# Optimization experiments

Measured on AMD Instinct MI355X. Metric: run time of the kernel, lower is better.

The kernel has to match this reference:

```python
import jax, jax.numpy as jnp
import numpy as np

N_NODES = 100000
N_EDGES = 1600000
D_IN = 128
D_HID = 128


def setup_inputs() -> dict:
    key = jax.random.key(0)
    ks = jax.random.split(key, 9)
    x = jax.random.normal(ks[0], (N_NODES, D_IN), dtype=jnp.float32)
    edge_index = jax.random.randint(ks[1], (2, N_EDGES), 0, N_NODES, dtype=jnp.int64)
    s = 1.0 / np.sqrt(D_IN)
    W0 = jax.random.uniform(ks[2], (D_IN, D_HID), jnp.float32, -s, s)
    W1 = jax.random.uniform(ks[3], (D_HID, D_HID), jnp.float32, -s, s)
    W2 = jax.random.uniform(ks[4], (D_HID, D_HID), jnp.float32, -s, s)
    b0 = jax.random.uniform(ks[5], (D_HID,), jnp.float32, -s, s)
    b1 = jax.random.uniform(ks[6], (D_HID,), jnp.float32, -s, s)
    b2 = jax.random.uniform(ks[7], (D_HID,), jnp.float32, -s, s)
    return {"x": x, "edge_index": edge_index,
            "W0": W0, "W1": W1, "W2": W2, "b0": b0, "b1": b1, "b2": b2}


def _gcn_norm(edge_index, num_nodes):
    # add self loops, compute symmetric normalization D^-1/2 (A+I) D^-1/2
    loop = jnp.arange(num_nodes, dtype=edge_index.dtype)
    src = jnp.concatenate([edge_index[0], loop])
    dst = jnp.concatenate([edge_index[1], loop])
    deg = jax.ops.segment_sum(jnp.ones_like(dst, dtype=jnp.float32), dst,
                              num_segments=num_nodes)
    dis = jnp.where(deg > 0, jax.lax.rsqrt(deg), 0.0)
    norm = dis[src] * dis[dst]  # [E+N]
    return src, dst, norm


def _gcn_conv(x, src, dst, norm, W, b, num_nodes):
    h = x @ W                           # [N, D]
    msg = h[src] * norm[:, None]        # [E+N, D]
    out = jax.ops.segment_sum(msg, dst, num_segments=num_nodes)
    return out + b


def reference(x, edge_index, W0, W1, W2, b0, b1, b2):
    n = x.shape[0]
    src, dst, norm = _gcn_norm(edge_index, n)
    h = jax.nn.relu(_gcn_conv(x, src, dst, norm, W0, b0, n))
    h = jax.nn.relu(_gcn_conv(h, src, dst, norm, W1, b1, n))
    h = jax.nn.relu(_gcn_conv(h, src, dst, norm, W2, b2, n))
    return jax.nn.log_softmax(h, axis=1)
```

## Files before the change

kernel.cpp:

```cpp
#include <hip/hip_runtime.h>
#include <cstdint>


#define D 128
#define NBMAX 800
#define ACHUNK 8192
#define QCAP 4608

typedef __attribute__((ext_vector_type(8))) short bf16x8;
typedef __attribute__((ext_vector_type(4))) float f32x4;

__device__ inline ushort f_to_bf(float f) {
    uint x = __float_as_uint(f);
    return (ushort)((x + 0x7fffu + ((x >> 16) & 1u)) >> 16);
}
__device__ inline uint pack_bf2(float a, float b) {
    return (uint)f_to_bf(a) | ((uint)f_to_bf(b) << 16);
}
__device__ inline float bf_lo(uint u) { return __uint_as_float(u << 16); }
__device__ inline float bf_hi(uint u) { return __uint_as_float(u & 0xffff0000u); }


__global__ void hist_pass(const int* __restrict__ ei, int* __restrict__ hist,
                          int* __restrict__ cursor, int E, int NB) {
    __shared__ int lh[NBMAX];
    if (blockIdx.x == 0 && threadIdx.x == 0) *cursor = 0;
    for (int i = threadIdx.x; i < NB; i += 256) lh[i] = 0;
    __syncthreads();
    int e0 = blockIdx.x * ACHUNK;
    int e1 = min(e0 + ACHUNK, E);
    for (int e = e0 + threadIdx.x; e < e1; e += 256)
        atomicAdd(&lh[ei[(size_t)E + e] >> 7], 1);
    __syncthreads();
    int* hrow = hist + (size_t)blockIdx.x * NB;
    for (int i = threadIdx.x; i < NB; i += 256) hrow[i] = lh[i];
}

__global__ void col_scan(int* __restrict__ hist, int* __restrict__ btotal,
                         int* __restrict__ bbase, int* __restrict__ cursor,
                         int B, int NB) {
    __shared__ int s[256];
    int g = blockIdx.x;
    int t = threadIdx.x;
    int v = (t < B) ? hist[(size_t)t * NB + g] : 0;
    s[t] = v;
    __syncthreads();
    for (int off = 1; off < 256; off <<= 1) {
        int u = (t >= off) ? s[t - off] : 0;
        __syncthreads();
        s[t] += u;
        __syncthreads();
    }
    if (t < B) hist[(size_t)t * NB + g] = s[t] - v;
    if (t == 255) {
        btotal[g] = s[255];
        bbase[g] = atomicAdd(cursor, s[255]);
    }
}

__global__ void scatter_pass(const int* __restrict__ ei, const int* __restrict__ hist,
                             const int* __restrict__ bbase, uint* __restrict__ queue,
                             int E, int NB) {
    __shared__ int loff[NBMAX];
    const int* hrow = hist + (size_t)blockIdx.x * NB;
    for (int i = threadIdx.x; i < NB; i += 256) loff[i] = bbase[i] + hrow[i];
    __syncthreads();
    int e0 = blockIdx.x * ACHUNK;
    int e1 = min(e0 + ACHUNK, E);
    for (int e = e0 + threadIdx.x; e < e1; e += 256) {
        int d = ei[(size_t)E + e];
        int s = ei[e];
        int slot = atomicAdd(&loff[d >> 7], 1);
        queue[slot] = ((uint)(d & 127) << 17) | (uint)s;
    }
}

__global__ void finalize_pass(const uint* __restrict__ queue, const int* __restrict__ bbase,
                              const int* __restrict__ btotal, int2* __restrict__ bd,
                              float* __restrict__ dis, int* __restrict__ col, int N) {
    __shared__ uint qs[QCAP];
    __shared__ int cnt[128], pre[128], run[128];
    int g = blockIdx.x;
    int t = threadIdx.x;
    int base = bbase[g], m = btotal[g];
    bool fits = (m <= QCAP);
    if (t < 128) { cnt[t] = 0; run[t] = 0; }
    __syncthreads();
    for (int i = t; i < m; i += 256) {
        uint e = queue[base + i];
        if (fits) qs[i] = e;
        atomicAdd(&cnt[e >> 17], 1);
    }
    __syncthreads();
    if (t < 128) pre[t] = cnt[t];
    __syncthreads();
    for (int off = 1; off < 128; off <<= 1) {
        int u = (t < 128 && t >= off) ? pre[t - off] : 0;
        __syncthreads();
        if (t < 128) pre[t] += u;
        __syncthreads();
    }
    if (t < 128) {
        int node = (g << 7) + t;
        if (node < N) {
            bd[node] = make_int2(base + pre[t] - cnt[t], cnt[t]);
            dis[node] = rsqrtf((float)(cnt[t] + 1));
        }
    }
    __syncthreads();
    for (int i = t; i < m; i += 256) {
        uint e = fits ? qs[i] : queue[base + i];
        int idx = (int)(e >> 17);
        int r = atomicAdd(&run[idx], 1);
        col[base + pre[idx] - cnt[idx] + r] = (int)(e & 0x1FFFFu);
    }
}

__global__ void convert_w3(const float* __restrict__ W0, const float* __restrict__ W1,
                           const float* __restrict__ W2, ushort* __restrict__ Wt0,
                           ushort* __restrict__ Wt1, ushort* __restrict__ Wt2) {
    int which = blockIdx.x >> 6;
    int i = (blockIdx.x & 63) * 256 + threadIdx.x;
    const float* W = which == 0 ? W0 : (which == 1 ? W1 : W2);
    ushort* Wt = which == 0 ? Wt0 : (which == 1 ? Wt1 : Wt2);
    int k = i >> 7, nn = i & 127;
    Wt[nn * D + k] = f_to_bf(W[i]);
}

template <int F32IN>
__global__ __launch_bounds__(256)
void gemm_mfma(const void* __restrict__ Xv, const ushort* __restrict__ Wt,
               const float* __restrict__ dis, ushort* __restrict__ G, int n) {
    __shared__ ushort Bs[32 * 64 * 8];
    int tid = threadIdx.x;
    int wave = tid >> 6, lane = tid & 63;
    int lr = lane & 15, quad = lane >> 4;
    int rowbase = blockIdx.x * 128 + wave * 32;

    for (int s = tid; s < 2048; s += 256) {
        int g = s >> 6, l = s & 63;
        int kk = g >> 3, nt = g & 7;
        int srow = nt * 16 + (l & 15);
        int scol = kk * 32 + (l >> 4) * 8;
        ((uint4*)Bs)[s] = *(const uint4*)(Wt + srow * D + scol);
    }
    __syncthreads();

    int ar0 = min(rowbase + lr, n - 1);
    int ar1 = min(rowbase + 16 + lr, n - 1);

    f32x4 acc[2][8];
#pragma unroll
    for (int rt = 0; rt < 2; rt++)
#pragma unroll
        for (int nt = 0; nt < 8; nt++) acc[rt][nt] = (f32x4){0.f, 0.f, 0.f, 0.f};

#pragma unroll
    for (int kk = 0; kk < 4; kk++) {
        bf16x8 a0, a1;
        if (F32IN) {
            const float* X = (const float*)Xv;
            const float* p0 = X + (size_t)ar0 * D + kk * 32 + quad * 8;
            const float* p1 = X + (size_t)ar1 * D + kk * 32 + quad * 8;
            float4 u0 = ((const float4*)p0)[0], v0 = ((const float4*)p0)[1];
            float4 u1 = ((const float4*)p1)[0], v1 = ((const float4*)p1)[1];
            a0 = (bf16x8){(short)f_to_bf(u0.x), (short)f_to_bf(u0.y), (short)f_to_bf(u0.z), (short)f_to_bf(u0.w),
                          (short)f_to_bf(v0.x), (short)f_to_bf(v0.y), (short)f_to_bf(v0.z), (short)f_to_bf(v0.w)};
            a1 = (bf16x8){(short)f_to_bf(u1.x), (short)f_to_bf(u1.y), (short)f_to_bf(u1.z), (short)f_to_bf(u1.w),
                          (short)f_to_bf(v1.x), (short)f_to_bf(v1.y), (short)f_to_bf(v1.z), (short)f_to_bf(v1.w)};
        } else {
            const ushort* X = (const ushort*)Xv;
            a0 = ((const bf16x8*)(X + (size_t)ar0 * D))[kk * 4 + quad];
            a1 = ((const bf16x8*)(X + (size_t)ar1 * D))[kk * 4 + quad];
        }
#pragma unroll
        for (int nt = 0; nt < 8; nt++) {
            bf16x8 b = ((const bf16x8*)Bs)[(kk * 8 + nt) * 64 + lane];
            acc[0][nt] = __builtin_amdgcn_mfma_f32_16x16x32_bf16(a0, b, acc[0][nt], 0, 0, 0);
            acc[1][nt] = __builtin_amdgcn_mfma_f32_16x16x32_bf16(a1, b, acc[1][nt], 0, 0, 0);
        }
    }

#pragma unroll
    for (int rt = 0; rt < 2; rt++) {
#pragma unroll
        for (int r = 0; r < 4; r++) {
            int row = rowbase + rt * 16 + quad * 4 + r;
            if (row < n) {
                float dsc = dis[row];
#pragma unroll
                for (int nt = 0; nt < 8; nt++)
                    G[(size_t)row * D + nt * 16 + lr] = f_to_bf(dsc * acc[rt][nt][r]);
            }
        }
    }
}

__global__ __launch_bounds__(256)
void agg_gemm(const ushort* __restrict__ Gv, const float* __restrict__ dis,
              const int2* __restrict__ bd, const int* __restrict__ col,
              const float* __restrict__ bias, const ushort* __restrict__ Wt,
              ushort* __restrict__ Gout, int n) {
    __shared__ ushort Bs[32 * 64 * 8];
    __shared__ ushort As[16 * 128];
    int tid = threadIdx.x;
    int r16 = tid >> 4;
    int lane16 = tid & 15;
    int node = blockIdx.x * 16 + r16;

    for (int s = tid; s < 2048; s += 256) {
        int g = s >> 6, l = s & 63;
        int kk = g >> 3, nt = g & 7;
        int srow = nt * 16 + (l & 15);
        int scol = kk * 32 + (l >> 4) * 8;
        ((uint4*)Bs)[s] = *(const uint4*)(Wt + srow * D + scol);
    }

    float a0 = 0.f, a1 = 0.f, a2 = 0.f, a3 = 0.f,
          a4 = 0.f, a5 = 0.f, a6 = 0.f, a7 = 0.f;
    if (node < n) {
        const uint4* base = (const uint4*)Gv;
        uint4 u = base[(size_t)node * 16 + lane16];
        a0 = bf_lo(u.x); a1 = bf_hi(u.x); a2 = bf_lo(u.y); a3 = bf_hi(u.y);
        a4 = bf_lo(u.z); a5 = bf_hi(u.z); a6 = bf_lo(u.w); a7 = bf_hi(u.w);

        int2 be = bd[node];
        int beg = be.x, end = be.x + be.y;
        int j = beg;
        for (; j + 8 <= end; j += 8) {
            uint4 v0 = base[(size_t)col[j + 0] * 16 + lane16];
            uint4 v1 = base[(size_t)col[j + 1] * 16 + lane16];
            uint4 v2 = base[(size_t)col[j + 2] * 16 + lane16];
            uint4 v3 = base[(size_t)col[j + 3] * 16 + lane16];
            uint4 v4 = base[(size_t)col[j + 4] * 16 + lane16];
            uint4 v5 = base[(size_t)col[j + 5] * 16 + lane16];
            uint4 v6 = base[(size_t)col[j + 6] * 16 + lane16];
            uint4 v7 = base[(size_t)col[j + 7] * 16 + lane16];
            a0 += bf_lo(v0.x) + bf_lo(v1.x) + bf_lo(v2.x) + bf_lo(v3.x)
                + bf_lo(v4.x) + bf_lo(v5.x) + bf_lo(v6.x) + bf_lo(v7.x);
            a1 += bf_hi(v0.x) + bf_hi(v1.x) + bf_hi(v2.x) + bf_hi(v3.x)
                + bf_hi(v4.x) + bf_hi(v5.x) + bf_hi(v6.x) + bf_hi(v7.x);
            a2 += bf_lo(v0.y) + bf_lo(v1.y) + bf_lo(v2.y) + bf_lo(v3.y)
                + bf_lo(v4.y) + bf_lo(v5.y) + bf_lo(v6.y) + bf_lo(v7.y);
            a3 += bf_hi(v0.y) + bf_hi(v1.y) + bf_hi(v2.y) + bf_hi(v3.y)
                + bf_hi(v4.y) + bf_hi(v5.y) + bf_hi(v6.y) + bf_hi(v7.y);
            a4 += bf_lo(v0.z) + bf_lo(v1.z) + bf_lo(v2.z) + bf_lo(v3.z)
                + bf_lo(v4.z) + bf_lo(v5.z) + bf_lo(v6.z) + bf_lo(v7.z);
            a5 += bf_hi(v0.z) + bf_hi(v1.z) + bf_hi(v2.z) + bf_hi(v3.z)
                + bf_hi(v4.z) + bf_hi(v5.z) + bf_hi(v6.z) + bf_hi(v7.z);
            a6 += bf_lo(v0.w) + bf_lo(v1.w) + bf_lo(v2.w) + bf_lo(v3.w)
                + bf_lo(v4.w) + bf_lo(v5.w) + bf_lo(v6.w) + bf_lo(v7.w);
            a7 += bf_hi(v0.w) + bf_hi(v1.w) + bf_hi(v2.w) + bf_hi(v3.w)
                + bf_hi(v4.w) + bf_hi(v5.w) + bf_hi(v6.w) + bf_hi(v7.w);
        }
        for (; j < end; j++) {
            uint4 v = base[(size_t)col[j] * 16 + lane16];
            a0 += bf_lo(v.x); a1 += bf_hi(v.x); a2 += bf_lo(v.y); a3 += bf_hi(v.y);
            a4 += bf_lo(v.z); a5 += bf_hi(v.z); a6 += bf_lo(v.w); a7 += bf_hi(v.w);
        }

        float di = dis[node];
        float4 bA = ((const float4*)bias)[lane16 * 2];
        float4 bB = ((const float4*)bias)[lane16 * 2 + 1];
        a0 = fmaxf(di * a0 + bA.x, 0.f); a1 = fmaxf(di * a1 + bA.y, 0.f);
        a2 = fmaxf(di * a2 + bA.z, 0.f); a3 = fmaxf(di * a3 + bA.w, 0.f);
        a4 = fmaxf(di * a4 + bB.x, 0.f); a5 = fmaxf(di * a5 + bB.y, 0.f);
        a6 = fmaxf(di * a6 + bB.z, 0.f); a7 = fmaxf(di * a7 + bB.w, 0.f);
    }

    {
        uint4 packed = make_uint4(pack_bf2(a0, a1), pack_bf2(a2, a3),
                                  pack_bf2(a4, a5), pack_bf2(a6, a7));
        uint woff = ((uint)(r16 * 256 + lane16 * 16)) ^ ((uint)(r16 & 7) << 4);
        *(uint4*)((char*)As + woff) = packed;
    }
    __syncthreads();

    int wave = tid >> 6, lane = tid & 63;
    int lr = lane & 15, quad = lane >> 4;
    f32x4 acc0 = (f32x4){0.f, 0.f, 0.f, 0.f};
    f32x4 acc1 = (f32x4){0.f, 0.f, 0.f, 0.f};
#pragma unroll
    for (int kk = 0; kk < 4; kk++) {
        uint roff = ((uint)(lr * 256 + (kk * 4 + quad) * 16)) ^ ((uint)(lr & 7) << 4);
        bf16x8 a = *(const bf16x8*)((const char*)As + roff);
        bf16x8 b0 = ((const bf16x8*)Bs)[(kk * 8 + wave * 2 + 0) * 64 + lane];
        bf16x8 b1 = ((const bf16x8*)Bs)[(kk * 8 + wave * 2 + 1) * 64 + lane];
        acc0 = __builtin_amdgcn_mfma_f32_16x16x32_bf16(a, b0, acc0, 0, 0, 0);
        acc1 = __builtin_amdgcn_mfma_f32_16x16x32_bf16(a, b1, acc1, 0, 0, 0);
    }

#pragma unroll
    for (int r = 0; r < 4; r++) {
        int row = blockIdx.x * 16 + quad * 4 + r;
        if (row < n) {
            float dsc = dis[row];
            Gout[(size_t)row * D + (wave * 2 + 0) * 16 + lr] = f_to_bf(dsc * acc0[r]);
            Gout[(size_t)row * D + (wave * 2 + 1) * 16 + lr] = f_to_bf(dsc * acc1[r]);
        }
    }
}

template <int MODE>
__global__ __launch_bounds__(256)
void aggregate(const ushort* __restrict__ Gv, const float* __restrict__ dis,
               const int2* __restrict__ bd, const int* __restrict__ col,
               const float* __restrict__ bias, void* __restrict__ outv, int n) {
    int node = blockIdx.x * 16 + (threadIdx.x >> 4);
    if (node >= n) return;
    int lane = threadIdx.x & 15;
    const uint4* base = (const uint4*)Gv;

    uint4 u = base[(size_t)node * 16 + lane];
    float a0 = bf_lo(u.x), a1 = bf_hi(u.x), a2 = bf_lo(u.y), a3 = bf_hi(u.y);
    float a4 = bf_lo(u.z), a5 = bf_hi(u.z), a6 = bf_lo(u.w), a7 = bf_hi(u.w);

    int2 be = bd[node];
    int beg = be.x, end = be.x + be.y;
    int j = beg;
    for (; j + 8 <= end; j += 8) {
        uint4 v0 = base[(size_t)col[j + 0] * 16 + lane];
        uint4 v1 = base[(size_t)col[j + 1] * 16 + lane];
        uint4 v2 = base[(size_t)col[j + 2] * 16 + lane];
        uint4 v3 = base[(size_t)col[j + 3] * 16 + lane];
        uint4 v4 = base[(size_t)col[j + 4] * 16 + lane];
        uint4 v5 = base[(size_t)col[j + 5] * 16 + lane];
        uint4 v6 = base[(size_t)col[j + 6] * 16 + lane];
        uint4 v7 = base[(size_t)col[j + 7] * 16 + lane];
        a0 += bf_lo(v0.x) + bf_lo(v1.x) + bf_lo(v2.x) + bf_lo(v3.x)
            + bf_lo(v4.x) + bf_lo(v5.x) + bf_lo(v6.x) + bf_lo(v7.x);
        a1 += bf_hi(v0.x) + bf_hi(v1.x) + bf_hi(v2.x) + bf_hi(v3.x)
            + bf_hi(v4.x) + bf_hi(v5.x) + bf_hi(v6.x) + bf_hi(v7.x);
        a2 += bf_lo(v0.y) + bf_lo(v1.y) + bf_lo(v2.y) + bf_lo(v3.y)
            + bf_lo(v4.y) + bf_lo(v5.y) + bf_lo(v6.y) + bf_lo(v7.y);
        a3 += bf_hi(v0.y) + bf_hi(v1.y) + bf_hi(v2.y) + bf_hi(v3.y)
            + bf_hi(v4.y) + bf_hi(v5.y) + bf_hi(v6.y) + bf_hi(v7.y);
        a4 += bf_lo(v0.z) + bf_lo(v1.z) + bf_lo(v2.z) + bf_lo(v3.z)
            + bf_lo(v4.z) + bf_lo(v5.z) + bf_lo(v6.z) + bf_lo(v7.z);
        a5 += bf_hi(v0.z) + bf_hi(v1.z) + bf_hi(v2.z) + bf_hi(v3.z)
            + bf_hi(v4.z) + bf_hi(v5.z) + bf_hi(v6.z) + bf_hi(v7.z);
        a6 += bf_lo(v0.w) + bf_lo(v1.w) + bf_lo(v2.w) + bf_lo(v3.w)
            + bf_lo(v4.w) + bf_lo(v5.w) + bf_lo(v6.w) + bf_lo(v7.w);
        a7 += bf_hi(v0.w) + bf_hi(v1.w) + bf_hi(v2.w) + bf_hi(v3.w)
            + bf_hi(v4.w) + bf_hi(v5.w) + bf_hi(v6.w) + bf_hi(v7.w);
    }
    for (; j < end; j++) {
        uint4 v = base[(size_t)col[j] * 16 + lane];
        a0 += bf_lo(v.x); a1 += bf_hi(v.x); a2 += bf_lo(v.y); a3 += bf_hi(v.y);
        a4 += bf_lo(v.z); a5 += bf_hi(v.z); a6 += bf_lo(v.w); a7 += bf_hi(v.w);
    }

    float di = dis[node];
    float4 bA = ((const float4*)bias)[lane * 2];
    float4 bB = ((const float4*)bias)[lane * 2 + 1];
    a0 = fmaxf(di * a0 + bA.x, 0.f); a1 = fmaxf(di * a1 + bA.y, 0.f);
    a2 = fmaxf(di * a2 + bA.z, 0.f); a3 = fmaxf(di * a3 + bA.w, 0.f);
    a4 = fmaxf(di * a4 + bB.x, 0.f); a5 = fmaxf(di * a5 + bB.y, 0.f);
    a6 = fmaxf(di * a6 + bB.z, 0.f); a7 = fmaxf(di * a7 + bB.w, 0.f);

    if (MODE == 1) {
        float m = fmaxf(fmaxf(fmaxf(a0, a1), fmaxf(a2, a3)),
                        fmaxf(fmaxf(a4, a5), fmaxf(a6, a7)));
        for (int off = 8; off > 0; off >>= 1) m = fmaxf(m, __shfl_xor(m, off, 16));
        float e = __expf(a0 - m) + __expf(a1 - m) + __expf(a2 - m) + __expf(a3 - m)
                + __expf(a4 - m) + __expf(a5 - m) + __expf(a6 - m) + __expf(a7 - m);
        for (int off = 8; off > 0; off >>= 1) e += __shfl_xor(e, off, 16);
        float ls = m + __logf(e);
        ((float4*)outv)[(size_t)node * 32 + lane * 2]     = make_float4(a0 - ls, a1 - ls, a2 - ls, a3 - ls);
        ((float4*)outv)[(size_t)node * 32 + lane * 2 + 1] = make_float4(a4 - ls, a5 - ls, a6 - ls, a7 - ls);
    } else {
        ((uint4*)outv)[(size_t)node * 16 + lane] =
            make_uint4(pack_bf2(a0, a1), pack_bf2(a2, a3), pack_bf2(a4, a5), pack_bf2(a6, a7));
    }
}


static inline size_t align256(size_t x) { return (x + 255) & ~(size_t)255; }

extern "C" void kernel_launch(void* const* d_in, const int* in_sizes, int n_in,
                              void* d_out, int out_size, void* d_ws, size_t ws_size,
                              hipStream_t stream) {
    const float* x  = (const float*)d_in[0];
    const int*   ei = (const int*)d_in[1];
    const float* W0 = (const float*)d_in[2];
    const float* W1 = (const float*)d_in[3];
    const float* W2 = (const float*)d_in[4];
    const float* b0 = (const float*)d_in[5];
    const float* b1 = (const float*)d_in[6];
    const float* b2 = (const float*)d_in[7];
    float* out      = (float*)d_out;

    const int N = in_sizes[0] / D;
    const int E = in_sizes[1] / 2;

    const int NB = (N + 127) >> 7;
    const int B  = (E + ACHUNK - 1) / ACHUNK;

    char* ws = (char*)d_ws;
    size_t off = 0;
    float*  dis      = (float*)(ws + off);  off = align256(off + (size_t)N * 4);
    int2*   bd       = (int2*)(ws + off);   off = align256(off + (size_t)N * 8);
    int*    hist     = (int*)(ws + off);    off = align256(off + (size_t)B * NB * 4);
    int*    btotal   = (int*)(ws + off);    off = align256(off + (size_t)NB * 4);
    int*    bbase    = (int*)(ws + off);    off = align256(off + (size_t)NB * 4);
    int*    cursor   = (int*)(ws + off);    off = align256(off + 4);
    ushort* Wt0      = (ushort*)(ws + off); off = align256(off + (size_t)D * D * 2);
    ushort* Wt1      = (ushort*)(ws + off); off = align256(off + (size_t)D * D * 2);
    ushort* Wt2      = (ushort*)(ws + off); off = align256(off + (size_t)D * D * 2);
    int*    col      = (int*)(ws + off);    off = align256(off + (size_t)E * 4);
    ushort* gA       = (ushort*)(ws + off); off = align256(off + (size_t)N * D * 2);
    ushort* gB       = (ushort*)(ws + off); off = align256(off + (size_t)N * D * 2);
    ushort* g0       = (ushort*)d_out;
    uint*   queue    = (uint*)gA;
    (void)ws_size;

    hist_pass<<<B, 256, 0, stream>>>(ei, hist, cursor, E, NB);
    col_scan<<<NB, 256, 0, stream>>>(hist, btotal, bbase, cursor, B, NB);
    scatter_pass<<<B, 256, 0, stream>>>(ei, hist, bbase, queue, E, NB);
    finalize_pass<<<NB, 256, 0, stream>>>(queue, bbase, btotal, bd, dis, col, N);

    convert_w3<<<192, 256, 0, stream>>>(W0, W1, W2, Wt0, Wt1, Wt2);

    const int gemmBlocks = (N + 127) / 128;
    const int fuseBlocks = (N + 15) / 16;

    gemm_mfma<1><<<gemmBlocks, 256, 0, stream>>>(x, Wt0, dis, g0, N);
    agg_gemm<<<fuseBlocks, 256, 0, stream>>>(g0, dis, bd, col, b0, Wt1, gA, N);
    agg_gemm<<<fuseBlocks, 256, 0, stream>>>(gA, dis, bd, col, b1, Wt2, gB, N);
    aggregate<1><<<fuseBlocks, 256, 0, stream>>>(gB, dis, bd, col, b2, out, N);
}
```

Measured before the change: 433.8 us.

## Read GEMM weights directly from global in agg_gemm, fix CSR build block count

The fused aggregate+GEMM kernel no longer stages the whole 32 KB weight matrix into LDS per 16-node block. Each MFMA lane now loads its B fragments straight from global memory, relying on L1/L2 caching, which removes per-block staging traffic and LDS pressure. The edge bucketing passes now use a fixed 256 chunks instead of a chunk size of 8192, matching the 256-wide column scan. Buffers are reassigned to ping-pong between two workspace arrays instead of writing intermediates into the output.

Measured after the change: 422.9 us. 1.03x faster.

```diff
diff --git a/kernel.cpp b/kernel.cpp
--- a/kernel.cpp
+++ b/kernel.cpp
@@ -4,8 +4,8 @@
 
 #define D 128
 #define NBMAX 800
-#define ACHUNK 8192
 #define QCAP 4608
+#define CB 256
 
 typedef __attribute__((ext_vector_type(8))) short bf16x8;
 typedef __attribute__((ext_vector_type(4))) float f32x4;
@@ -27,8 +27,8 @@
     if (blockIdx.x == 0 && threadIdx.x == 0) *cursor = 0;
     for (int i = threadIdx.x; i < NB; i += 256) lh[i] = 0;
     __syncthreads();
-    int e0 = blockIdx.x * ACHUNK;
-    int e1 = min(e0 + ACHUNK, E);
+    int CE = (E + CB - 1) / CB;
+    int e0 = blockIdx.x * CE, e1 = min(e0 + CE, E);
     for (int e = e0 + threadIdx.x; e < e1; e += 256)
         atomicAdd(&lh[ei[(size_t)E + e] >> 7], 1);
     __syncthreads();
@@ -37,12 +37,10 @@
 }
 
 __global__ void col_scan(int* __restrict__ hist, int* __restrict__ btotal,
-                         int* __restrict__ bbase, int* __restrict__ cursor,
-                         int B, int NB) {
+                         int* __restrict__ bbase, int* __restrict__ cursor, int NB) {
     __shared__ int s[256];
-    int g = blockIdx.x;
-    int t = threadIdx.x;
-    int v = (t < B) ? hist[(size_t)t * NB + g] : 0;
+    int g = blockIdx.x, t = threadIdx.x;
+    int v = hist[(size_t)t * NB + g];
     s[t] = v;
     __syncthreads();
     for (int off = 1; off < 256; off <<= 1) {
@@ -51,11 +49,8 @@
         s[t] += u;
         __syncthreads();
     }
-    if (t < B) hist[(size_t)t * NB + g] = s[t] - v;
-    if (t == 255) {
-        btotal[g] = s[255];
-        bbase[g] = atomicAdd(cursor, s[255]);
-    }
+    hist[(size_t)t * NB + g] = s[t] - v;
+    if (t == 255) { btotal[g] = s[255]; bbase[g] = atomicAdd(cursor, s[255]); }
 }
 
 __global__ void scatter_pass(const int* __restrict__ ei, const int* __restrict__ hist,
@@ -65,8 +60,8 @@
     const int* hrow = hist + (size_t)blockIdx.x * NB;
     for (int i = threadIdx.x; i < NB; i += 256) loff[i] = bbase[i] + hrow[i];
     __syncthreads();
-    int e0 = blockIdx.x * ACHUNK;
-    int e1 = min(e0 + ACHUNK, E);
+    int CE = (E + CB - 1) / CB;
+    int e0 = blockIdx.x * CE, e1 = min(e0 + CE, E);
     for (int e = e0 + threadIdx.x; e < e1; e += 256) {
         int d = ei[(size_t)E + e];
         int s = ei[e];
@@ -80,8 +75,7 @@
                               float* __restrict__ dis, int* __restrict__ col, int N) {
     __shared__ uint qs[QCAP];
     __shared__ int cnt[128], pre[128], run[128];
-    int g = blockIdx.x;
-    int t = threadIdx.x;
+    int g = blockIdx.x, t = threadIdx.x;
     int base = bbase[g], m = btotal[g];
     bool fits = (m <= QCAP);
     if (t < 128) { cnt[t] = 0; run[t] = 0; }
@@ -201,20 +195,10 @@
               const int2* __restrict__ bd, const int* __restrict__ col,
               const float* __restrict__ bias, const ushort* __restrict__ Wt,
               ushort* __restrict__ Gout, int n) {
-    __shared__ ushort Bs[32 * 64 * 8];
     __shared__ ushort As[16 * 128];
     int tid = threadIdx.x;
-    int r16 = tid >> 4;
-    int lane16 = tid & 15;
+    int r16 = tid >> 4, lane16 = tid & 15;
     int node = blockIdx.x * 16 + r16;
-
-    for (int s = tid; s < 2048; s += 256) {
-        int g = s >> 6, l = s & 63;
-        int kk = g >> 3, nt = g & 7;
-        int srow = nt * 16 + (l & 15);
-        int scol = kk * 32 + (l >> 4) * 8;
-        ((uint4*)Bs)[s] = *(const uint4*)(Wt + srow * D + scol);
-    }
 
     float a0 = 0.f, a1 = 0.f, a2 = 0.f, a3 = 0.f,
           a4 = 0.f, a5 = 0.f, a6 = 0.f, a7 = 0.f;
@@ -280,12 +264,14 @@
     int lr = lane & 15, quad = lane >> 4;
     f32x4 acc0 = (f32x4){0.f, 0.f, 0.f, 0.f};
     f32x4 acc1 = (f32x4){0.f, 0.f, 0.f, 0.f};
+    const ushort* wb0 = Wt + ((wave * 2 + 0) * 16 + lr) * D + quad * 8;
+    const ushort* wb1 = Wt + ((wave * 2 + 1) * 16 + lr) * D + quad * 8;
 #pragma unroll
     for (int kk = 0; kk < 4; kk++) {
         uint roff = ((uint)(lr * 256 + (kk * 4 + quad) * 16)) ^ ((uint)(lr & 7) << 4);
         bf16x8 a = *(const bf16x8*)((const char*)As + roff);
-        bf16x8 b0 = ((const bf16x8*)Bs)[(kk * 8 + wave * 2 + 0) * 64 + lane];
-        bf16x8 b1 = ((const bf16x8*)Bs)[(kk * 8 + wave * 2 + 1) * 64 + lane];
+        bf16x8 b0 = *(const bf16x8*)(wb0 + kk * 32);
+        bf16x8 b1 = *(const bf16x8*)(wb1 + kk * 32);
         acc0 = __builtin_amdgcn_mfma_f32_16x16x32_bf16(a, b0, acc0, 0, 0, 0);
         acc1 = __builtin_amdgcn_mfma_f32_16x16x32_bf16(a, b1, acc1, 0, 0, 0);
     }
@@ -392,15 +378,13 @@
 
     const int N = in_sizes[0] / D;
     const int E = in_sizes[1] / 2;
-
     const int NB = (N + 127) >> 7;
-    const int B  = (E + ACHUNK - 1) / ACHUNK;
 
     char* ws = (char*)d_ws;
     size_t off = 0;
     float*  dis      = (float*)(ws + off);  off = align256(off + (size_t)N * 4);
     int2*   bd       = (int2*)(ws + off);   off = align256(off + (size_t)N * 8);
-    int*    hist     = (int*)(ws + off);    off = align256(off + (size_t)B * NB * 4);
+    int*    hist     = (int*)(ws + off);    off = align256(off + (size_t)CB * NB * 4);
     int*    btotal   = (int*)(ws + off);    off = align256(off + (size_t)NB * 4);
     int*    bbase    = (int*)(ws + off);    off = align256(off + (size_t)NB * 4);
     int*    cursor   = (int*)(ws + off);    off = align256(off + 4);
@@ -408,15 +392,14 @@
     ushort* Wt1      = (ushort*)(ws + off); off = align256(off + (size_t)D * D * 2);
     ushort* Wt2      = (ushort*)(ws + off); off = align256(off + (size_t)D * D * 2);
     int*    col      = (int*)(ws + off);    off = align256(off + (size_t)E * 4);
-    ushort* gA       = (ushort*)(ws + off); off = align256(off + (size_t)N * D * 2);
-    ushort* gB       = (ushort*)(ws + off); off = align256(off + (size_t)N * D * 2);
-    ushort* g0       = (ushort*)d_out;
-    uint*   queue    = (uint*)gA;
+    ushort* bufA     = (ushort*)(ws + off); off = align256(off + (size_t)N * D * 2);
+    ushort* bufB     = (ushort*)(ws + off); off = align256(off + (size_t)N * D * 2);
+    uint*   queue    = (uint*)bufB;
     (void)ws_size;
 
-    hist_pass<<<B, 256, 0, stream>>>(ei, hist, cursor, E, NB);
-    col_scan<<<NB, 256, 0, stream>>>(hist, btotal, bbase, cursor, B, NB);
-    scatter_pass<<<B, 256, 0, stream>>>(ei, hist, bbase, queue, E, NB);
+    hist_pass<<<CB, 256, 0, stream>>>(ei, hist, cursor, E, NB);
+    col_scan<<<NB, 256, 0, stream>>>(hist, btotal, bbase, cursor, NB);
+    scatter_pass<<<CB, 256, 0, stream>>>(ei, hist, bbase, queue, E, NB);
     finalize_pass<<<NB, 256, 0, stream>>>(queue, bbase, btotal, bd, dis, col, N);
 
     convert_w3<<<192, 256, 0, stream>>>(W0, W1, W2, Wt0, Wt1, Wt2);
@@ -424,8 +407,8 @@
     const int gemmBlocks = (N + 127) / 128;
     const int fuseBlocks = (N + 15) / 16;
 
-    gemm_mfma<1><<<gemmBlocks, 256, 0, stream>>>(x, Wt0, dis, g0, N);
-    agg_gemm<<<fuseBlocks, 256, 0, stream>>>(g0, dis, bd, col, b0, Wt1, gA, N);
-    agg_gemm<<<fuseBlocks, 256, 0, stream>>>(gA, dis, bd, col, b1, Wt2, gB, N);
-    aggregate<1><<<fuseBlocks, 256, 0, stream>>>(gB, dis, bd, col, b2, out, N);
-}
+    gemm_mfma<1><<<gemmBlocks, 256, 0, stream>>>(x, Wt0, dis, bufA, N);
+    agg_gemm<<<fuseBlocks, 256, 0, stream>>>(bufA, dis, bd, col, b0, Wt1, bufB, N);
+    agg_gemm<<<fuseBlocks, 256, 0, stream>>>(bufB, dis, bd, col, b1, Wt2, bufA, N);
+    aggregate<1><<<fuseBlocks, 256, 0, stream>>>(bufA, dis, bd, col, b2, out, N);
+}
```
